# Optimization experiments

Measured on AMD Instinct MI355X. Metric: run time of the kernel, lower is better.

## Reference

```python
import jax, jax.numpy as jnp
import numpy as np

UNITS = 2048

def _cat_complex(Wr, Wi):
    # real-matrix representation of complex matmul: [[Wr, -Wi], [Wi, Wr]]
    top = jnp.concatenate([Wr, -Wi], axis=-1)
    bot = jnp.concatenate([Wi, Wr], axis=-1)
    return jnp.concatenate([top, bot], axis=0)

def _hard_sigmoid(x):
    return jnp.clip(0.2 * x + 0.5, 0.0, 1.0)

def setup_inputs() -> dict:
    key = jax.random.key(0)
    ks = jax.random.split(key, 8)
    B, IN2, U3 = 1024, 4096, 3 * UNITS
    s_in = 1.0 / np.sqrt(IN2)
    s_h = 1.0 / np.sqrt(2 * UNITS)
    return {
        "inputs": jax.random.normal(ks[0], (B, IN2), jnp.float32),
        "h_tm1": jax.random.normal(ks[1], (B, 2 * UNITS), jnp.float32),
        "real_kernel": jax.random.normal(ks[2], (IN2 // 2, U3), jnp.float32) * s_in,
        "imaginary_kernel": jax.random.normal(ks[3], (IN2 // 2, U3), jnp.float32) * s_in,
        "real_recurrent_kernel": jax.random.normal(ks[4], (UNITS, U3), jnp.float32) * s_h,
        "imaginary_recurrent_kernel": jax.random.normal(ks[5], (UNITS, U3), jnp.float32) * s_h,
        "real_bias": jax.random.normal(ks[6], (U3,), jnp.float32) * 0.01,
        "imaginary_bias": jax.random.normal(ks[7], (U3,), jnp.float32) * 0.01,
    }

def reference(inputs, h_tm1, real_kernel, imaginary_kernel,
              real_recurrent_kernel, imaginary_recurrent_kernel,
              real_bias, imaginary_bias):
    u = UNITS
    # per-gate complex kernels in real [[Wr,-Wi],[Wi,Wr]] form
    Kz = _cat_complex(real_kernel[:, :u], imaginary_kernel[:, :u])
    Kr = _cat_complex(real_kernel[:, u:2 * u], imaginary_kernel[:, u:2 * u])
    Kh = _cat_complex(real_kernel[:, 2 * u:], imaginary_kernel[:, 2 * u:])
    Rz = _cat_complex(real_recurrent_kernel[:, :u], imaginary_recurrent_kernel[:, :u])
    Rr = _cat_complex(real_recurrent_kernel[:, u:2 * u], imaginary_recurrent_kernel[:, u:2 * u])
    Rh = _cat_complex(real_recurrent_kernel[:, 2 * u:], imaginary_recurrent_kernel[:, 2 * u:])
    bz = jnp.concatenate([real_bias[:u], imaginary_bias[:u]])
    br = jnp.concatenate([real_bias[u:2 * u], imaginary_bias[u:2 * u]])
    bh = jnp.concatenate([real_bias[2 * u:], imaginary_bias[2 * u:]])
    # implementation=1, reset_after=False, no dropout
    x_z = inputs @ Kz + bz
    x_r = inputs @ Kr + br
    x_h = inputs @ Kh + bh
    z = _hard_sigmoid(x_z + h_tm1 @ Rz)
    r = _hard_sigmoid(x_r + h_tm1 @ Rr)
    hh = jnp.tanh(x_h + (r * h_tm1) @ Rh)
    h = z * h_tm1 + (1.0 - z) * hh
    return h
```

## Files before the change

### kernel.cpp

```cpp
#include <hip/hip_runtime.h>

typedef _Float16 half8  __attribute__((ext_vector_type(8)));
typedef _Float16 half4v __attribute__((ext_vector_type(4)));
typedef _Float16 half2v __attribute__((ext_vector_type(2)));
typedef float    float4v __attribute__((ext_vector_type(4)));

__device__ __forceinline__ float hsig(float x) {
  return fminf(fmaxf(fmaf(x, 0.2f, 0.5f), 0.0f), 1.0f);
}

__global__ __launch_bounds__(256) void cvt_pair(const float* __restrict__ src,
                                                _Float16* __restrict__ d1,
                                                _Float16* __restrict__ d2) {
  int i = blockIdx.x * blockDim.x + threadIdx.x;
  int base = i * 4;
  int j = base & 4095;
  float s = (j < 2048) ? -1.0f : 1.0f;
  float4 v = *(const float4*)&src[base];
  half4v h1 = {(_Float16)v.x, (_Float16)v.y, (_Float16)v.z, (_Float16)v.w};
  half4v h2 = {(_Float16)(s * v.x), (_Float16)(s * v.y), (_Float16)(s * v.z), (_Float16)(s * v.w)};
  *(half4v*)&d1[base] = h1;
  *(half4v*)&d2[base] = h2;
}

__global__ __launch_bounds__(256) void transpose_cast(
    const float* __restrict__ s0, const float* __restrict__ s1,
    const float* __restrict__ s2, const float* __restrict__ s3,
    _Float16* __restrict__ d0, _Float16* __restrict__ d1m,
    _Float16* __restrict__ d2m, _Float16* __restrict__ d3m)
{
  __shared__ float tile[64][65];
  const float* srcs[4] = {s0, s1, s2, s3};
  _Float16*    dsts[4] = {d0, d1m, d2m, d3m};
  const float* src = srcs[blockIdx.z];
  _Float16*    dst = dsts[blockIdx.z];

  const int tid = threadIdx.x;
  const int k0 = blockIdx.x * 64;
  const int j0 = blockIdx.y * 64;

  const int tx = tid & 63, ty = tid >> 6;
#pragma unroll
  for (int r = 0; r < 64; r += 4)
    tile[r + ty][tx] = src[(size_t)(k0 + r + ty) * 6144 + j0 + tx];
  __syncthreads();

  const int txk = (tid & 31) * 2;
  const int tyn = tid >> 5;
#pragma unroll
  for (int r = 0; r < 64; r += 8) {
    int jl = r + tyn;
    half2v p = {(_Float16)tile[txk][jl], (_Float16)tile[txk + 1][jl]};
    *(half2v*)&dst[(size_t)(j0 + jl) * 2048 + k0 + txk] = p;
  }
}

__global__ __launch_bounds__(256) void rgate(const _Float16* __restrict__ xacc,
                                             const float* __restrict__ h,
                                             _Float16* __restrict__ A1r,
                                             _Float16* __restrict__ A2r) {
  int i = blockIdx.x * blockDim.x + threadIdx.x;
  int base = i * 4;
  int m = base >> 12;
  int j = base & 4095;
  float s = (j < 2048) ? -1.0f : 1.0f;
  half4v rp = *(const half4v*)&xacc[(size_t)m * 12288 + 4096 + j];
  float4 hv = *(const float4*)&h[base];
  float p0 = hsig((float)rp[0]) * hv.x;
  float p1 = hsig((float)rp[1]) * hv.y;
  float p2 = hsig((float)rp[2]) * hv.z;
  float p3 = hsig((float)rp[3]) * hv.w;
  half4v o1 = {(_Float16)p0, (_Float16)p1, (_Float16)p2, (_Float16)p3};
  half4v o2 = {(_Float16)(s * p0), (_Float16)(s * p1), (_Float16)(s * p2), (_Float16)(s * p3)};
  *(half4v*)&A1r[base] = o1;
  *(half4v*)&A2r[base] = o2;
}

__global__ __launch_bounds__(256) void combine(const _Float16* __restrict__ xacc,
                                               const _Float16* __restrict__ P0,
                                               const _Float16* __restrict__ P1,
                                               const float* __restrict__ h,
                                               float* __restrict__ out) {
  int i = blockIdx.x * blockDim.x + threadIdx.x;
  int base = i * 4;
  int m = base >> 12;
  int j = base & 4095;
  half4v zv = *(const half4v*)&xacc[(size_t)m * 12288 + j];
  half4v xh = *(const half4v*)&xacc[(size_t)m * 12288 + 8192 + j];
  half4v p0 = *(const half4v*)&P0[base];
  half4v p1 = *(const half4v*)&P1[base];
  float4 hv = *(const float4*)&h[base];
  float4 o;
  {
    float z = hsig((float)zv[0]); float t = tanhf((float)xh[0] + (float)p0[0] + (float)p1[0]);
    o.x = z * hv.x + (1.0f - z) * t;
  }
  {
    float z = hsig((float)zv[1]); float t = tanhf((float)xh[1] + (float)p0[1] + (float)p1[1]);
    o.y = z * hv.y + (1.0f - z) * t;
  }
  {
    float z = hsig((float)zv[2]); float t = tanhf((float)xh[2] + (float)p0[2] + (float)p1[2]);
    o.z = z * hv.z + (1.0f - z) * t;
  }
  {
    float z = hsig((float)zv[3]); float t = tanhf((float)xh[3] + (float)p0[3] + (float)p1[3]);
    o.w = z * hv.w + (1.0f - z) * t;
  }
  *(float4*)&out[base] = o;
}

template<int FINAL>
__global__ __launch_bounds__(256, 3) void gemm_big(
    const _Float16* __restrict__ Ax1, const _Float16* __restrict__ Ax2,
    const _Float16* __restrict__ Ah1, const _Float16* __restrict__ Ah2,
    const _Float16* __restrict__ WKr, const _Float16* __restrict__ WKi,
    const _Float16* __restrict__ WRr, const _Float16* __restrict__ WRi,
    _Float16* __restrict__ xacc,
    _Float16* __restrict__ P0, _Float16* __restrict__ P1,
    const float* __restrict__ rbias, const float* __restrict__ ibias)
{
  __shared__ __align__(16) _Float16 lds[16384];
  const int tid  = threadIdx.x;
  const int lane = tid & 63;
  const int wave = tid >> 6;
  const int quad = lane >> 4;
  const int r16  = lane & 15;
  const int wm = (wave >> 1) * 64;
  const int wn = (wave & 1) * 64;
  const int mbase = blockIdx.y * 128;
  const int nbase = blockIdx.x * 128;

  const int  gate   = nbase >> 12;
  const bool hi     = (nbase & 2048) != 0;
  const int  jprime = nbase & 2047;

  int nph;
  const _Float16* pA[4];
  const _Float16* pB[4];
  if (FINAL) {
    nph = 1;
    const _Float16* Ax = hi ? Ax2 : Ax1;
    const _Float16* BL = hi ? WKi : WKr;
    const _Float16* BH = hi ? WKr : WKi;
    if (blockIdx.z == 0) {
      pA[0] = Ax + (size_t)mbase * 4096;
      pB[0] = BL + (size_t)jprime * 2048;
    } else {
      pA[0] = Ax + (size_t)mbase * 4096 + 2048;
      pB[0] = BH + (size_t)jprime * 2048;
    }
  } else {
    const size_t browK = (size_t)(gate * 2048 + jprime) * 2048;
    const _Float16* Ax = hi ? Ax2 : Ax1;
    const _Float16* KL = hi ? WKi : WKr;
    const _Float16* KH = hi ? WKr : WKi;
    pA[0] = Ax + (size_t)mbase * 4096;      pB[0] = KL + browK;
    pA[1] = pA[0] + 2048;                   pB[1] = KH + browK;
    if (gate < 2) {
      nph = 4;
      const _Float16* Ah = hi ? Ah2 : Ah1;
      const _Float16* RL = hi ? WRi : WRr;
      const _Float16* RH = hi ? WRr : WRi;
      pA[2] = Ah + (size_t)mbase * 4096;    pB[2] = RL + browK;
      pA[3] = pA[2] + 2048;                 pB[3] = RH + browK;
    } else {
      nph = 2;
    }
  }

  float4v acc[4][4];
#pragma unroll
  for (int i = 0; i < 4; ++i)
#pragma unroll
    for (int j = 0; j < 4; ++j) acc[i][j] = (float4v){0.f, 0.f, 0.f, 0.f};

  int offA[4], offB[4], ldsA[4], ldsB[4];
#pragma unroll
  for (int i = 0; i < 4; ++i) {
    int c = i * 256 + tid;
    int row = c >> 3;
    int sw = (c & 7) ^ (row & 7);
    offA[i] = row * 4096 + sw * 8;
    offB[i] = row * 2048 + sw * 8;
    ldsA[i] = c * 8;
    ldsB[i] = 8192 + c * 8;
  }

#pragma unroll 1
  for (int p = 0; p < 4; ++p) {
    if (p >= nph) break;
    const _Float16* Ab = pA[p];
    const _Float16* Bb = pB[p];
#pragma unroll 1
    for (int it = 0; it < 32; ++it) {
#pragma unroll
      for (int i = 0; i < 4; ++i)
        __builtin_amdgcn_global_load_lds(
            (__attribute__((address_space(1))) void*)(Ab + offA[i]),
            (__attribute__((address_space(3))) void*)&lds[ldsA[i]], 16, 0, 0);
#pragma unroll
      for (int i = 0; i < 4; ++i)
        __builtin_amdgcn_global_load_lds(
            (__attribute__((address_space(1))) void*)(Bb + offB[i]),
            (__attribute__((address_space(3))) void*)&lds[ldsB[i]], 16, 0, 0);
      Ab += 64;
      Bb += 64;
      __syncthreads();
#pragma unroll
      for (int ks = 0; ks < 2; ++ks) {
        half8 af[4], bf[4];
        int akg = ks * 4 + quad;
#pragma unroll
        for (int t = 0; t < 4; ++t) {
          int arow = wm + t * 16 + r16;
          af[t] = *(const half8*)&lds[(arow * 8 + (akg ^ (arow & 7))) * 8];
          int brow = wn + t * 16 + r16;
          bf[t] = *(const half8*)&lds[8192 + (brow * 8 + (akg ^ (brow & 7))) * 8];
        }
#pragma unroll
        for (int mt = 0; mt < 4; ++mt)
#pragma unroll
          for (int nt = 0; nt < 4; ++nt)
            acc[mt][nt] = __builtin_amdgcn_mfma_f32_16x16x32_f16(af[mt], bf[nt], acc[mt][nt], 0, 0, 0);
      }
      __syncthreads();
    }
  }

  const int mrow0 = mbase + wm + quad * 4;
  const int ncol0 = nbase + wn + r16;
  if (!FINAL) {
#pragma unroll
    for (int nt = 0; nt < 4; ++nt) {
      int n = ncol0 + nt * 16;
      int g = n >> 12, j = n & 4095;
      float b = (j < 2048) ? rbias[g * 2048 + j] : ibias[g * 2048 + j - 2048];
#pragma unroll
      for (int mt = 0; mt < 4; ++mt)
#pragma unroll
        for (int e = 0; e < 4; ++e) {
          int m = mrow0 + mt * 16 + e;
          xacc[(size_t)m * 12288 + n] = (_Float16)(acc[mt][nt][e] + b);
        }
    }
  } else {
    _Float16* P = blockIdx.z ? P1 : P0;
#pragma unroll
    for (int nt = 0; nt < 4; ++nt) {
      int n = ncol0 + nt * 16;
#pragma unroll
      for (int mt = 0; mt < 4; ++mt)
#pragma unroll
        for (int e = 0; e < 4; ++e) {
          int m = mrow0 + mt * 16 + e;
          P[(size_t)m * 4096 + n] = (_Float16)acc[mt][nt][e];
        }
    }
  }
}

extern "C" void kernel_launch(void* const* d_in, const int* in_sizes, int n_in,
                              void* d_out, int out_size, void* d_ws, size_t ws_size,
                              hipStream_t stream) {
  const float* inputs = (const float*)d_in[0];
  const float* h_tm1  = (const float*)d_in[1];
  const float* rk     = (const float*)d_in[2];
  const float* ik     = (const float*)d_in[3];
  const float* rrk    = (const float*)d_in[4];
  const float* irk    = (const float*)d_in[5];
  const float* rb     = (const float*)d_in[6];
  const float* ib     = (const float*)d_in[7];
  float* out = (float*)d_out;

  char* ws = (char*)d_ws;
  _Float16* WrK  = (_Float16*)(ws + 0);
  _Float16* WiK  = (_Float16*)(ws + 25165824);
  _Float16* WrR  = (_Float16*)(ws + 50331648);
  _Float16* WiR  = (_Float16*)(ws + 75497472);
  _Float16* A1x  = (_Float16*)(ws + 100663296);
  _Float16* A2x  = (_Float16*)(ws + 109051904);
  _Float16* A1h  = (_Float16*)(ws + 117440512);
  _Float16* A2h  = (_Float16*)(ws + 125829120);
  _Float16* xacc = (_Float16*)(ws + 134217728);
  _Float16* A1r  = A1x;
  _Float16* A2r  = A2x;
  _Float16* P0   = A1h;
  _Float16* P1   = A2h;

  cvt_pair<<<4096, 256, 0, stream>>>(inputs, A1x, A2x);
  cvt_pair<<<4096, 256, 0, stream>>>(h_tm1, A1h, A2h);
  transpose_cast<<<dim3(32, 96, 4), 256, 0, stream>>>(rk, ik, rrk, irk, WrK, WiK, WrR, WiR);
  gemm_big<0><<<dim3(96, 8), 256, 0, stream>>>(A1x, A2x, A1h, A2h, WrK, WiK, WrR, WiR,
                                               xacc, nullptr, nullptr, rb, ib);
  rgate<<<4096, 256, 0, stream>>>(xacc, h_tm1, A1r, A2r);
  gemm_big<1><<<dim3(32, 8, 2), 256, 0, stream>>>(A1r, A2r, nullptr, nullptr,
                                                  WrR + (size_t)4096 * 2048,
                                                  WiR + (size_t)4096 * 2048,
                                                  nullptr, nullptr, nullptr, P0, P1,
                                                  nullptr, nullptr);
  combine<<<4096, 256, 0, stream>>>(xacc, P0, P1, h_tm1, out);
}
```

Baseline: 512.9 us.

## Replace first fused GEMM with 128x256-tile 512-thread kernel using direct-to-LDS loads

Adds a new gemm256 kernel for the input-plus-recurrent z/r/h GEMM. It uses 128x256 output tiles with 8 waves and a 4-buffer LDS ring filled by global_load_lds with two stages in flight, and raises MFMA wave priority. The larger tiles cut the grid from 96x8 to 48x8 blocks and increase operand reuse per tile. In exchange it needs 96KB of dynamic LDS per block, which limits occupancy, and the ring and waitcnt logic is handwritten.

```diff
diff --git a/kernel.cpp b/kernel.cpp
--- a/kernel.cpp
+++ b/kernel.cpp
@@ -108,6 +108,144 @@
     o.w = z * hv.w + (1.0f - z) * t;
   }
   *(float4*)&out[base] = o;
+}
+
+__global__ __launch_bounds__(512, 2) void gemm256(
+    const _Float16* __restrict__ Ax1, const _Float16* __restrict__ Ax2,
+    const _Float16* __restrict__ Ah1, const _Float16* __restrict__ Ah2,
+    const _Float16* __restrict__ WKr, const _Float16* __restrict__ WKi,
+    const _Float16* __restrict__ WRr, const _Float16* __restrict__ WRi,
+    _Float16* __restrict__ xacc,
+    const float* __restrict__ rbias, const float* __restrict__ ibias)
+{
+  extern __shared__ __align__(16) _Float16 smem[];
+  const int tid  = threadIdx.x;
+  const int lane = tid & 63;
+  const int wave = tid >> 6;
+  const int quad = lane >> 4;
+  const int r16  = lane & 15;
+  const int wm = (wave >> 2) * 64;
+  const int wn = (wave & 3) * 64;
+  const int mbase = blockIdx.y * 128;
+  const int nbase = blockIdx.x * 256;
+
+  const int  gate   = nbase >> 12;
+  const bool hi     = (nbase & 2048) != 0;
+  const int  jprime = nbase & 2047;
+
+  int nph;
+  const _Float16 *pA0, *pA1, *pA2, *pA3;
+  const _Float16 *pB0, *pB1, *pB2, *pB3;
+  {
+    const size_t browK = (size_t)(gate * 2048 + jprime) * 2048;
+    const _Float16* Ax = hi ? Ax2 : Ax1;
+    const _Float16* KL = hi ? WKi : WKr;
+    const _Float16* KH = hi ? WKr : WKi;
+    pA0 = Ax + (size_t)mbase * 4096;      pB0 = KL + browK;
+    pA1 = pA0 + 2048;                     pB1 = KH + browK;
+    if (gate < 2) {
+      nph = 4;
+      const _Float16* Ah = hi ? Ah2 : Ah1;
+      const _Float16* RL = hi ? WRi : WRr;
+      const _Float16* RH = hi ? WRr : WRi;
+      pA2 = Ah + (size_t)mbase * 4096;    pB2 = RL + browK;
+      pA3 = pA2 + 2048;                   pB3 = RH + browK;
+    } else {
+      nph = 2;
+      pA2 = pA0; pB2 = pB0; pA3 = pA0; pB3 = pB0;
+    }
+  }
+  const int NS = nph * 64;
+
+  const int arow_s = tid >> 2;
+  const int ag     = (tid & 3) ^ ((arow_s ^ (arow_s >> 2)) & 3);
+  const size_t aoff = (size_t)arow_s * 4096 + ag * 8;
+  const int aldsd   = tid * 8;
+
+  const int brow_s0 = tid >> 2;
+  const int bg0     = (tid & 3) ^ ((brow_s0 ^ (brow_s0 >> 2)) & 3);
+  const size_t boff0 = (size_t)brow_s0 * 2048 + bg0 * 8;
+  const int bldsd0   = tid * 8;
+  const int brow_s1 = brow_s0 + 128;
+  const int bg1     = (tid & 3) ^ ((brow_s1 ^ (brow_s1 >> 2)) & 3);
+  const size_t boff1 = (size_t)brow_s1 * 2048 + bg1 * 8;
+  const int bldsd1   = (tid + 512) * 8;
+
+#define STAGE(S2) do {                                                          \
+    int p2_ = (S2) >> 6;                                                        \
+    int kof_ = ((S2) & 63) * 32;                                                \
+    int bb_ = (S2) & 3;                                                         \
+    const _Float16* As_ = p2_ == 0 ? pA0 : p2_ == 1 ? pA1 : p2_ == 2 ? pA2 : pA3; \
+    const _Float16* Bs_ = p2_ == 0 ? pB0 : p2_ == 1 ? pB1 : p2_ == 2 ? pB2 : pB3; \
+    __builtin_amdgcn_global_load_lds(                                           \
+        (__attribute__((address_space(1))) void*)(As_ + aoff + kof_),           \
+        (__attribute__((address_space(3))) void*)&smem[bb_ * 4096 + aldsd], 16, 0, 0); \
+    __builtin_amdgcn_global_load_lds(                                           \
+        (__attribute__((address_space(1))) void*)(Bs_ + boff0 + kof_),          \
+        (__attribute__((address_space(3))) void*)&smem[16384 + bb_ * 8192 + bldsd0], 16, 0, 0); \
+    __builtin_amdgcn_global_load_lds(                                           \
+        (__attribute__((address_space(1))) void*)(Bs_ + boff1 + kof_),          \
+        (__attribute__((address_space(3))) void*)&smem[16384 + bb_ * 8192 + bldsd1], 16, 0, 0); \
+  } while (0)
+
+  float4v acc[4][4];
+#pragma unroll
+  for (int i = 0; i < 4; ++i)
+#pragma unroll
+    for (int j = 0; j < 4; ++j) acc[i][j] = (float4v){0.f, 0.f, 0.f, 0.f};
+
+  STAGE(0);
+  STAGE(1);
+
+#pragma unroll 1
+  for (int s = 0; s < NS; ++s) {
+    if (s + 2 < NS) {
+      STAGE(s + 2);
+      asm volatile("s_waitcnt vmcnt(6)" ::: "memory");
+    } else if (s + 1 < NS) {
+      asm volatile("s_waitcnt vmcnt(3)" ::: "memory");
+    } else {
+      asm volatile("s_waitcnt vmcnt(0)" ::: "memory");
+    }
+    __builtin_amdgcn_s_barrier();
+    asm volatile("" ::: "memory");
+
+    const int b = s & 3;
+    half8 af[4], bf[4];
+#pragma unroll
+    for (int t = 0; t < 4; ++t) {
+      int arow = wm + t * 16 + r16;
+      af[t] = *(const half8*)&smem[b * 4096 +
+                 (arow * 4 + (quad ^ ((arow ^ (arow >> 2)) & 3))) * 8];
+      int brow = wn + t * 16 + r16;
+      bf[t] = *(const half8*)&smem[16384 + b * 8192 +
+                 (brow * 4 + (quad ^ ((brow ^ (brow >> 2)) & 3))) * 8];
+    }
+    __builtin_amdgcn_s_setprio(1);
+#pragma unroll
+    for (int mt = 0; mt < 4; ++mt)
+#pragma unroll
+      for (int nt = 0; nt < 4; ++nt)
+        acc[mt][nt] = __builtin_amdgcn_mfma_f32_16x16x32_f16(af[mt], bf[nt], acc[mt][nt], 0, 0, 0);
+    __builtin_amdgcn_s_setprio(0);
+  }
+#undef STAGE
+
+  const int mrow0 = mbase + wm + quad * 4;
+  const int ncol0 = nbase + wn + r16;
+#pragma unroll
+  for (int nt = 0; nt < 4; ++nt) {
+    int n = ncol0 + nt * 16;
+    int g = n >> 12, j = n & 4095;
+    float bia = (j < 2048) ? rbias[g * 2048 + j] : ibias[g * 2048 + j - 2048];
+#pragma unroll
+    for (int mt = 0; mt < 4; ++mt)
+#pragma unroll
+      for (int e = 0; e < 4; ++e) {
+        int m = mrow0 + mt * 16 + e;
+        xacc[(size_t)m * 12288 + n] = (_Float16)(acc[mt][nt][e] + bia);
+      }
+  }
 }
 
 template<int FINAL>
@@ -291,8 +429,8 @@
   cvt_pair<<<4096, 256, 0, stream>>>(inputs, A1x, A2x);
   cvt_pair<<<4096, 256, 0, stream>>>(h_tm1, A1h, A2h);
   transpose_cast<<<dim3(32, 96, 4), 256, 0, stream>>>(rk, ik, rrk, irk, WrK, WiK, WrR, WiR);
-  gemm_big<0><<<dim3(96, 8), 256, 0, stream>>>(A1x, A2x, A1h, A2h, WrK, WiK, WrR, WiR,
-                                               xacc, nullptr, nullptr, rb, ib);
+  gemm256<<<dim3(48, 8), 512, 98304, stream>>>(A1x, A2x, A1h, A2h, WrK, WiK, WrR, WiR,
+                                               xacc, rb, ib);
   rgate<<<4096, 256, 0, stream>>>(xacc, h_tm1, A1r, A2r);
   gemm_big<1><<<dim3(32, 8, 2), 256, 0, stream>>>(A1r, A2r, nullptr, nullptr,
                                                   WrR + (size_t)4096 * 2048,
```

Result: slower. 611.0 us (+19.1%).

## Use Gauss three-multiplication complex matmul with split-K recurrent GEMM

Applied to the files above, without the earlier changes.

The four-real-GEMM complex product becomes Gauss's three-product form. Prep kernels build (r-i), (r+i) and i weight planes and r, i, r+i activation planes, and each GEMM tile runs three K-phases. The shared product is kept in fp16 registers and folded into both the real and imaginary outputs. The aim is to cut MFMA work by about a quarter; the fp16 stash and the extra sums add rounding error. The candidate GEMM is also split four ways over K with partial outputs summed in the combine kernel, and workgroup IDs are remapped for locality.

```diff
diff --git a/kernel.cpp b/kernel.cpp
--- a/kernel.cpp
+++ b/kernel.cpp
@@ -9,117 +9,149 @@
   return fminf(fmaxf(fmaf(x, 0.2f, 0.5f), 0.0f), 1.0f);
 }
 
-__global__ __launch_bounds__(256) void cvt_pair(const float* __restrict__ src,
-                                                _Float16* __restrict__ d1,
-                                                _Float16* __restrict__ d2) {
-  int i = blockIdx.x * blockDim.x + threadIdx.x;
+__device__ __forceinline__ half2v pk2(float a, float b) {
+  half2v r; r[0] = (_Float16)a; r[1] = (_Float16)b; return r;
+}
+
+
+__global__ __launch_bounds__(256) void prep_a(const float* __restrict__ x,
+                                              const float* __restrict__ h,
+                                              _Float16* __restrict__ PXr, _Float16* __restrict__ PXi,
+                                              _Float16* __restrict__ PXs, _Float16* __restrict__ PHr,
+                                              _Float16* __restrict__ PHi, _Float16* __restrict__ PHs) {
+  int i = blockIdx.x * 256 + threadIdx.x;
+  const float* src; _Float16 *Pr, *Pi, *Ps;
+  if (blockIdx.y == 0) { src = x; Pr = PXr; Pi = PXi; Ps = PXs; }
+  else                 { src = h; Pr = PHr; Pi = PHi; Ps = PHs; }
   int base = i * 4;
-  int j = base & 4095;
-  float s = (j < 2048) ? -1.0f : 1.0f;
-  float4 v = *(const float4*)&src[base];
-  half4v h1 = {(_Float16)v.x, (_Float16)v.y, (_Float16)v.z, (_Float16)v.w};
-  half4v h2 = {(_Float16)(s * v.x), (_Float16)(s * v.y), (_Float16)(s * v.z), (_Float16)(s * v.w)};
-  *(half4v*)&d1[base] = h1;
-  *(half4v*)&d2[base] = h2;
-}
-
-__global__ __launch_bounds__(256) void transpose_cast(
-    const float* __restrict__ s0, const float* __restrict__ s1,
-    const float* __restrict__ s2, const float* __restrict__ s3,
-    _Float16* __restrict__ d0, _Float16* __restrict__ d1m,
-    _Float16* __restrict__ d2m, _Float16* __restrict__ d3m)
-{
-  __shared__ float tile[64][65];
-  const float* srcs[4] = {s0, s1, s2, s3};
-  _Float16*    dsts[4] = {d0, d1m, d2m, d3m};
-  const float* src = srcs[blockIdx.z];
-  _Float16*    dst = dsts[blockIdx.z];
-
+  int m = base >> 11, j = base & 2047;
+  float4 a  = *(const float4*)&src[(size_t)m * 4096 + j];
+  float4 bv = *(const float4*)&src[(size_t)m * 4096 + 2048 + j];
+  size_t o = (size_t)m * 2048 + j;
+  half4v hr, hi2, hs;
+  hr[0]=(_Float16)a.x;  hr[1]=(_Float16)a.y;  hr[2]=(_Float16)a.z;  hr[3]=(_Float16)a.w;
+  hi2[0]=(_Float16)bv.x; hi2[1]=(_Float16)bv.y; hi2[2]=(_Float16)bv.z; hi2[3]=(_Float16)bv.w;
+  hs[0]=(_Float16)(a.x+bv.x); hs[1]=(_Float16)(a.y+bv.y);
+  hs[2]=(_Float16)(a.z+bv.z); hs[3]=(_Float16)(a.w+bv.w);
+  *(half4v*)&Pr[o] = hr;
+  *(half4v*)&Pi[o] = hi2;
+  *(half4v*)&Ps[o] = hs;
+}
+
+__global__ __launch_bounds__(256) void transpose_cast3(
+    const float* __restrict__ rkK, const float* __restrict__ ikK,
+    const float* __restrict__ rkR, const float* __restrict__ ikR,
+    _Float16* __restrict__ WdK, _Float16* __restrict__ WsK, _Float16* __restrict__ WiK,
+    _Float16* __restrict__ WdR, _Float16* __restrict__ WsR, _Float16* __restrict__ WiR) {
+  __shared__ float tr[64][65];
+  __shared__ float ti[64][65];
+  const float* rs  = blockIdx.z ? rkR : rkK;
+  const float* is2 = blockIdx.z ? ikR : ikK;
+  _Float16* Wd = blockIdx.z ? WdR : WdK;
+  _Float16* Ws = blockIdx.z ? WsR : WsK;
+  _Float16* Wi = blockIdx.z ? WiR : WiK;
   const int tid = threadIdx.x;
   const int k0 = blockIdx.x * 64;
   const int j0 = blockIdx.y * 64;
-
   const int tx = tid & 63, ty = tid >> 6;
 #pragma unroll
-  for (int r = 0; r < 64; r += 4)
-    tile[r + ty][tx] = src[(size_t)(k0 + r + ty) * 6144 + j0 + tx];
+  for (int r = 0; r < 64; r += 4) {
+    size_t so = (size_t)(k0 + r + ty) * 6144 + j0 + tx;
+    tr[r + ty][tx] = rs[so];
+    ti[r + ty][tx] = is2[so];
+  }
   __syncthreads();
-
   const int txk = (tid & 31) * 2;
   const int tyn = tid >> 5;
 #pragma unroll
   for (int r = 0; r < 64; r += 8) {
     int jl = r + tyn;
-    half2v p = {(_Float16)tile[txk][jl], (_Float16)tile[txk + 1][jl]};
-    *(half2v*)&dst[(size_t)(j0 + jl) * 2048 + k0 + txk] = p;
-  }
-}
-
-__global__ __launch_bounds__(256) void rgate(const _Float16* __restrict__ xacc,
-                                             const float* __restrict__ h,
-                                             _Float16* __restrict__ A1r,
-                                             _Float16* __restrict__ A2r) {
-  int i = blockIdx.x * blockDim.x + threadIdx.x;
-  int base = i * 4;
-  int m = base >> 12;
-  int j = base & 4095;
-  float s = (j < 2048) ? -1.0f : 1.0f;
-  half4v rp = *(const half4v*)&xacc[(size_t)m * 12288 + 4096 + j];
-  float4 hv = *(const float4*)&h[base];
-  float p0 = hsig((float)rp[0]) * hv.x;
-  float p1 = hsig((float)rp[1]) * hv.y;
-  float p2 = hsig((float)rp[2]) * hv.z;
-  float p3 = hsig((float)rp[3]) * hv.w;
-  half4v o1 = {(_Float16)p0, (_Float16)p1, (_Float16)p2, (_Float16)p3};
-  half4v o2 = {(_Float16)(s * p0), (_Float16)(s * p1), (_Float16)(s * p2), (_Float16)(s * p3)};
-  *(half4v*)&A1r[base] = o1;
-  *(half4v*)&A2r[base] = o2;
-}
-
-__global__ __launch_bounds__(256) void combine(const _Float16* __restrict__ xacc,
-                                               const _Float16* __restrict__ P0,
-                                               const _Float16* __restrict__ P1,
-                                               const float* __restrict__ h,
-                                               float* __restrict__ out) {
-  int i = blockIdx.x * blockDim.x + threadIdx.x;
-  int base = i * 4;
-  int m = base >> 12;
-  int j = base & 4095;
-  half4v zv = *(const half4v*)&xacc[(size_t)m * 12288 + j];
-  half4v xh = *(const half4v*)&xacc[(size_t)m * 12288 + 8192 + j];
-  half4v p0 = *(const half4v*)&P0[base];
-  half4v p1 = *(const half4v*)&P1[base];
-  float4 hv = *(const float4*)&h[base];
-  float4 o;
-  {
-    float z = hsig((float)zv[0]); float t = tanhf((float)xh[0] + (float)p0[0] + (float)p1[0]);
-    o.x = z * hv.x + (1.0f - z) * t;
-  }
-  {
-    float z = hsig((float)zv[1]); float t = tanhf((float)xh[1] + (float)p0[1] + (float)p1[1]);
-    o.y = z * hv.y + (1.0f - z) * t;
-  }
-  {
-    float z = hsig((float)zv[2]); float t = tanhf((float)xh[2] + (float)p0[2] + (float)p1[2]);
-    o.z = z * hv.z + (1.0f - z) * t;
-  }
-  {
-    float z = hsig((float)zv[3]); float t = tanhf((float)xh[3] + (float)p0[3] + (float)p1[3]);
-    o.w = z * hv.w + (1.0f - z) * t;
-  }
-  *(float4*)&out[base] = o;
-}
-
-template<int FINAL>
-__global__ __launch_bounds__(256, 3) void gemm_big(
-    const _Float16* __restrict__ Ax1, const _Float16* __restrict__ Ax2,
-    const _Float16* __restrict__ Ah1, const _Float16* __restrict__ Ah2,
-    const _Float16* __restrict__ WKr, const _Float16* __restrict__ WKi,
-    const _Float16* __restrict__ WRr, const _Float16* __restrict__ WRi,
-    _Float16* __restrict__ xacc,
+    float r0 = tr[txk][jl], r1 = tr[txk + 1][jl];
+    float i0 = ti[txk][jl], i1 = ti[txk + 1][jl];
+    size_t dof = (size_t)(j0 + jl) * 2048 + k0 + txk;
+    *(half2v*)&Wd[dof] = pk2(r0 - i0, r1 - i1);
+    *(half2v*)&Ws[dof] = pk2(r0 + i0, r1 + i1);
+    *(half2v*)&Wi[dof] = pk2(i0, i1);
+  }
+}
+
+__device__ __forceinline__ void run_phase(const _Float16* Ab, const _Float16* Bb, int nit,
+                                          _Float16* lds, int tid, int wm, int wn,
+                                          int quad, int r16, float4v (&acc)[4][4]) {
+  int off[4], ldsA[4], ldsB[4];
+#pragma unroll
+  for (int i = 0; i < 4; ++i) {
+    int c = i * 256 + tid;
+    int row = c >> 3;
+    int sw = (c & 7) ^ (row & 7);
+    off[i]  = row * 2048 + sw * 8;
+    ldsA[i] = c * 8;
+    ldsB[i] = 8192 + c * 8;
+  }
+#pragma unroll 1
+  for (int it = 0; it < nit; ++it) {
+#pragma unroll
+    for (int i = 0; i < 4; ++i)
+      __builtin_amdgcn_global_load_lds(
+          (__attribute__((address_space(1))) void*)(Ab + off[i]),
+          (__attribute__((address_space(3))) void*)&lds[ldsA[i]], 16, 0, 0);
+#pragma unroll
+    for (int i = 0; i < 4; ++i)
+      __builtin_amdgcn_global_load_lds(
+          (__attribute__((address_space(1))) void*)(Bb + off[i]),
+          (__attribute__((address_space(3))) void*)&lds[ldsB[i]], 16, 0, 0);
+    Ab += 64;
+    Bb += 64;
+    __syncthreads();
+#pragma unroll
+    for (int ks = 0; ks < 2; ++ks) {
+      half8 af[4], bf[4];
+      int akg = ks * 4 + quad;
+#pragma unroll
+      for (int t = 0; t < 4; ++t) {
+        int arow = wm + t * 16 + r16;
+        af[t] = *(const half8*)&lds[(arow * 8 + (akg ^ (arow & 7))) * 8];
+        int brow = wn + t * 16 + r16;
+        bf[t] = *(const half8*)&lds[8192 + (brow * 8 + (akg ^ (brow & 7))) * 8];
+      }
+#pragma unroll
+      for (int mt = 0; mt < 4; ++mt)
+#pragma unroll
+        for (int nt = 0; nt < 4; ++nt)
+          acc[mt][nt] = __builtin_amdgcn_mfma_f32_16x16x32_f16(af[mt], bf[nt], acc[mt][nt], 0, 0, 0);
+    }
+    __syncthreads();
+  }
+}
+
+__device__ __forceinline__ void write_tile(_Float16* __restrict__ dst, int ldc, int colbase,
+    int mrow0, int ncol0, const float4v (&acc)[4][4], const half2v (&stash)[4][4][2],
+    float ssign, const float* __restrict__ bias, int bbase) {
+#pragma unroll
+  for (int nt = 0; nt < 4; ++nt) {
+    int nl = ncol0 + nt * 16;
+    float bv = bias ? bias[bbase + nl] : 0.0f;
+#pragma unroll
+    for (int mt = 0; mt < 4; ++mt)
+#pragma unroll
+      for (int e = 0; e < 4; ++e) {
+        float sv = (float)stash[mt][nt][e >> 1][e & 1];
+        int m = mrow0 + mt * 16 + e;
+        dst[(size_t)m * ldc + colbase + nl] = (_Float16)(acc[mt][nt][e] + ssign * sv + bv);
+      }
+  }
+}
+
+template<int MODE>
+__global__ __launch_bounds__(256, 3) void gemm_gauss(
+    const _Float16* __restrict__ WdK, const _Float16* __restrict__ WsK, const _Float16* __restrict__ WiK,
+    const _Float16* __restrict__ WdR, const _Float16* __restrict__ WsR, const _Float16* __restrict__ WiR,
+    const _Float16* __restrict__ PXr, const _Float16* __restrict__ PXi, const _Float16* __restrict__ PXs,
+    const _Float16* __restrict__ PHr, const _Float16* __restrict__ PHi, const _Float16* __restrict__ PHs,
+    _Float16* __restrict__ xaccX, _Float16* __restrict__ xaccH,
     _Float16* __restrict__ P0, _Float16* __restrict__ P1,
-    const float* __restrict__ rbias, const float* __restrict__ ibias)
-{
+    _Float16* __restrict__ P2, _Float16* __restrict__ P3,
+    const float* __restrict__ rbias, const float* __restrict__ ibias) {
   __shared__ __align__(16) _Float16 lds[16384];
   const int tid  = threadIdx.x;
   const int lane = tid & 63;
@@ -128,136 +160,161 @@
   const int r16  = lane & 15;
   const int wm = (wave >> 1) * 64;
   const int wn = (wave & 1) * 64;
-  const int mbase = blockIdx.y * 128;
-  const int nbase = blockIdx.x * 128;
-
-  const int  gate   = nbase >> 12;
-  const bool hi     = (nbase & 2048) != 0;
-  const int  jprime = nbase & 2047;
-
-  int nph;
-  const _Float16* pA[4];
-  const _Float16* pB[4];
-  if (FINAL) {
-    nph = 1;
-    const _Float16* Ax = hi ? Ax2 : Ax1;
-    const _Float16* BL = hi ? WKi : WKr;
-    const _Float16* BH = hi ? WKr : WKi;
-    if (blockIdx.z == 0) {
-      pA[0] = Ax + (size_t)mbase * 4096;
-      pB[0] = BL + (size_t)jprime * 2048;
+
+  const int NWG = MODE ? 512 : 640;
+  int b = blockIdx.x;
+  int wid = (b & 7) * (NWG >> 3) + (b >> 3);
+
+  int gate, jb, row, nit;
+  const _Float16 *A0, *A1, *A2, *B0, *B1, *B2;
+  _Float16* dst; int ldc, colRe, bbase;
+  const float *rb2, *ib2;
+
+  if (MODE == 0) {
+    nit = 32;
+    int side;
+    if (wid < 512) { gate = wid >> 8; side = (wid >> 7) & 1; jb = (wid >> 3) & 15; row = wid & 7; }
+    else { int t = wid - 512; gate = 2; side = 0; jb = (t >> 3) & 15; row = t & 7; }
+    size_t boff = (size_t)(gate * 2048 + jb * 128) * 2048;
+    size_t aoff = (size_t)(row * 128) * 2048;
+    if (side == 0) {
+      A0 = PXs + aoff; A1 = PXr + aoff; A2 = PXi + aoff;
+      B0 = WiK + boff; B1 = WdK + boff; B2 = WsK + boff;
+      dst = xaccX; ldc = 12288;
+      rb2 = rbias; ib2 = ibias;
     } else {
-      pA[0] = Ax + (size_t)mbase * 4096 + 2048;
-      pB[0] = BH + (size_t)jprime * 2048;
+      A0 = PHs + aoff; A1 = PHr + aoff; A2 = PHi + aoff;
+      B0 = WiR + boff; B1 = WdR + boff; B2 = WsR + boff;
+      dst = xaccH; ldc = 8192;
+      rb2 = nullptr; ib2 = nullptr;
     }
+    colRe = gate * 4096 + jb * 128;
+    bbase = gate * 2048 + jb * 128;
   } else {
-    const size_t browK = (size_t)(gate * 2048 + jprime) * 2048;
-    const _Float16* Ax = hi ? Ax2 : Ax1;
-    const _Float16* KL = hi ? WKi : WKr;
-    const _Float16* KH = hi ? WKr : WKi;
-    pA[0] = Ax + (size_t)mbase * 4096;      pB[0] = KL + browK;
-    pA[1] = pA[0] + 2048;                   pB[1] = KH + browK;
-    if (gate < 2) {
-      nph = 4;
-      const _Float16* Ah = hi ? Ah2 : Ah1;
-      const _Float16* RL = hi ? WRi : WRr;
-      const _Float16* RH = hi ? WRr : WRi;
-      pA[2] = Ah + (size_t)mbase * 4096;    pB[2] = RL + browK;
-      pA[3] = pA[2] + 2048;                 pB[3] = RH + browK;
-    } else {
-      nph = 2;
+    nit = 8;
+    int z = wid >> 7; int t = wid & 127;
+    jb = (t >> 3) & 15; row = t & 7;
+    int koff = z * 512;
+    size_t boff = (size_t)(4096 + jb * 128) * 2048 + koff;
+    size_t aoff = (size_t)(row * 128) * 2048 + koff;
+    A0 = PXs + aoff; A1 = PXr + aoff; A2 = PXi + aoff;
+    B0 = WiR + boff; B1 = WdR + boff; B2 = WsR + boff;
+    dst = (z == 0) ? P0 : (z == 1) ? P1 : (z == 2) ? P2 : P3;
+    ldc = 4096; colRe = jb * 128; bbase = 0;
+    gate = 0; rb2 = nullptr; ib2 = nullptr;
+  }
+
+  float4v acc[4][4];
+#pragma unroll
+  for (int i = 0; i < 4; ++i)
+#pragma unroll
+    for (int j = 0; j < 4; ++j) acc[i][j] = (float4v){0.f, 0.f, 0.f, 0.f};
+
+  run_phase(A0, B0, nit, lds, tid, wm, wn, quad, r16, acc);
+  half2v stash[4][4][2];
+#pragma unroll
+  for (int mt = 0; mt < 4; ++mt)
+#pragma unroll
+    for (int nt = 0; nt < 4; ++nt) {
+      stash[mt][nt][0] = pk2(acc[mt][nt][0], acc[mt][nt][1]);
+      stash[mt][nt][1] = pk2(acc[mt][nt][2], acc[mt][nt][3]);
+      acc[mt][nt] = (float4v){0.f, 0.f, 0.f, 0.f};
     }
-  }
-
-  float4v acc[4][4];
-#pragma unroll
-  for (int i = 0; i < 4; ++i)
-#pragma unroll
-    for (int j = 0; j < 4; ++j) acc[i][j] = (float4v){0.f, 0.f, 0.f, 0.f};
-
-  int offA[4], offB[4], ldsA[4], ldsB[4];
-#pragma unroll
-  for (int i = 0; i < 4; ++i) {
-    int c = i * 256 + tid;
-    int row = c >> 3;
-    int sw = (c & 7) ^ (row & 7);
-    offA[i] = row * 4096 + sw * 8;
-    offB[i] = row * 2048 + sw * 8;
-    ldsA[i] = c * 8;
-    ldsB[i] = 8192 + c * 8;
-  }
-
-#pragma unroll 1
-  for (int p = 0; p < 4; ++p) {
-    if (p >= nph) break;
-    const _Float16* Ab = pA[p];
-    const _Float16* Bb = pB[p];
-#pragma unroll 1
-    for (int it = 0; it < 32; ++it) {
-#pragma unroll
-      for (int i = 0; i < 4; ++i)
-        __builtin_amdgcn_global_load_lds(
-            (__attribute__((address_space(1))) void*)(Ab + offA[i]),
-            (__attribute__((address_space(3))) void*)&lds[ldsA[i]], 16, 0, 0);
-#pragma unroll
-      for (int i = 0; i < 4; ++i)
-        __builtin_amdgcn_global_load_lds(
-            (__attribute__((address_space(1))) void*)(Bb + offB[i]),
-            (__attribute__((address_space(3))) void*)&lds[ldsB[i]], 16, 0, 0);
-      Ab += 64;
-      Bb += 64;
-      __syncthreads();
-#pragma unroll
-      for (int ks = 0; ks < 2; ++ks) {
-        half8 af[4], bf[4];
-        int akg = ks * 4 + quad;
-#pragma unroll
-        for (int t = 0; t < 4; ++t) {
-          int arow = wm + t * 16 + r16;
-          af[t] = *(const half8*)&lds[(arow * 8 + (akg ^ (arow & 7))) * 8];
-          int brow = wn + t * 16 + r16;
-          bf[t] = *(const half8*)&lds[8192 + (brow * 8 + (akg ^ (brow & 7))) * 8];
-        }
-#pragma unroll
-        for (int mt = 0; mt < 4; ++mt)
-#pragma unroll
-          for (int nt = 0; nt < 4; ++nt)
-            acc[mt][nt] = __builtin_amdgcn_mfma_f32_16x16x32_f16(af[mt], bf[nt], acc[mt][nt], 0, 0, 0);
-      }
-      __syncthreads();
-    }
-  }
-
-  const int mrow0 = mbase + wm + quad * 4;
-  const int ncol0 = nbase + wn + r16;
-  if (!FINAL) {
-#pragma unroll
-    for (int nt = 0; nt < 4; ++nt) {
-      int n = ncol0 + nt * 16;
-      int g = n >> 12, j = n & 4095;
-      float b = (j < 2048) ? rbias[g * 2048 + j] : ibias[g * 2048 + j - 2048];
-#pragma unroll
-      for (int mt = 0; mt < 4; ++mt)
-#pragma unroll
-        for (int e = 0; e < 4; ++e) {
-          int m = mrow0 + mt * 16 + e;
-          xacc[(size_t)m * 12288 + n] = (_Float16)(acc[mt][nt][e] + b);
-        }
-    }
-  } else {
-    _Float16* P = blockIdx.z ? P1 : P0;
-#pragma unroll
-    for (int nt = 0; nt < 4; ++nt) {
-      int n = ncol0 + nt * 16;
-#pragma unroll
-      for (int mt = 0; mt < 4; ++mt)
-#pragma unroll
-        for (int e = 0; e < 4; ++e) {
-          int m = mrow0 + mt * 16 + e;
-          P[(size_t)m * 4096 + n] = (_Float16)acc[mt][nt][e];
-        }
-    }
-  }
+
+  const int mrow0 = row * 128 + wm + quad * 4;
+  const int ncol0 = wn + r16;
+
+  run_phase(A1, B1, nit, lds, tid, wm, wn, quad, r16, acc);
+  write_tile(dst, ldc, colRe, mrow0, ncol0, acc, stash, 1.0f, rb2, bbase);
+
+#pragma unroll
+  for (int mt = 0; mt < 4; ++mt)
+#pragma unroll
+    for (int nt = 0; nt < 4; ++nt) acc[mt][nt] = (float4v){0.f, 0.f, 0.f, 0.f};
+
+  run_phase(A2, B2, nit, lds, tid, wm, wn, quad, r16, acc);
+  write_tile(dst, ldc, colRe + 2048, mrow0, ncol0, acc, stash, -1.0f, ib2, bbase);
+}
+
+__global__ __launch_bounds__(256) void rgate3(const _Float16* __restrict__ xaccX,
+                                              const _Float16* __restrict__ xaccH,
+                                              const float* __restrict__ h,
+                                              _Float16* __restrict__ PRr,
+                                              _Float16* __restrict__ PRi,
+                                              _Float16* __restrict__ PRs) {
+  int i = blockIdx.x * 256 + threadIdx.x;
+  int base = i * 4;
+  int m = base >> 11, j = base & 2047;
+  half4v a1 = *(const half4v*)&xaccX[(size_t)m * 12288 + 4096 + j];
+  half4v a2 = *(const half4v*)&xaccH[(size_t)m * 8192 + 4096 + j];
+  half4v b1 = *(const half4v*)&xaccX[(size_t)m * 12288 + 4096 + 2048 + j];
+  half4v b2 = *(const half4v*)&xaccH[(size_t)m * 8192 + 4096 + 2048 + j];
+  float4 h1 = *(const float4*)&h[(size_t)m * 4096 + j];
+  float4 h2 = *(const float4*)&h[(size_t)m * 4096 + 2048 + j];
+  float p1[4], p2[4];
+  p1[0] = hsig((float)a1[0] + (float)a2[0]) * h1.x;
+  p1[1] = hsig((float)a1[1] + (float)a2[1]) * h1.y;
+  p1[2] = hsig((float)a1[2] + (float)a2[2]) * h1.z;
+  p1[3] = hsig((float)a1[3] + (float)a2[3]) * h1.w;
+  p2[0] = hsig((float)b1[0] + (float)b2[0]) * h2.x;
+  p2[1] = hsig((float)b1[1] + (float)b2[1]) * h2.y;
+  p2[2] = hsig((float)b1[2] + (float)b2[2]) * h2.z;
+  p2[3] = hsig((float)b1[3] + (float)b2[3]) * h2.w;
+  size_t o = (size_t)m * 2048 + j;
+  half4v orr, oi, os;
+#pragma unroll
+  for (int e = 0; e < 4; ++e) {
+    orr[e] = (_Float16)p1[e];
+    oi[e]  = (_Float16)p2[e];
+    os[e]  = (_Float16)(p1[e] + p2[e]);
+  }
+  *(half4v*)&PRr[o] = orr;
+  *(half4v*)&PRi[o] = oi;
+  *(half4v*)&PRs[o] = os;
+}
+
+__global__ __launch_bounds__(256) void combine4(const _Float16* __restrict__ xaccX,
+                                                const _Float16* __restrict__ xaccH,
+                                                const _Float16* __restrict__ P0,
+                                                const _Float16* __restrict__ P1,
+                                                const _Float16* __restrict__ P2,
+                                                const _Float16* __restrict__ P3,
+                                                const float* __restrict__ h,
+                                                float* __restrict__ out) {
+  int i = blockIdx.x * 256 + threadIdx.x;
+  int base = i * 4;
+  int m = base >> 12;
+  int j = base & 4095;
+  half4v zx = *(const half4v*)&xaccX[(size_t)m * 12288 + j];
+  half4v zh = *(const half4v*)&xaccH[(size_t)m * 8192 + j];
+  half4v xh = *(const half4v*)&xaccX[(size_t)m * 12288 + 8192 + j];
+  half4v p0 = *(const half4v*)&P0[base];
+  half4v p1 = *(const half4v*)&P1[base];
+  half4v p2 = *(const half4v*)&P2[base];
+  half4v p3 = *(const half4v*)&P3[base];
+  float4 hv = *(const float4*)&h[base];
+  float4 o;
+  {
+    float z = hsig((float)zx[0] + (float)zh[0]);
+    float t = tanhf((float)xh[0] + (float)p0[0] + (float)p1[0] + (float)p2[0] + (float)p3[0]);
+    o.x = z * hv.x + (1.0f - z) * t;
+  }
+  {
+    float z = hsig((float)zx[1] + (float)zh[1]);
+    float t = tanhf((float)xh[1] + (float)p0[1] + (float)p1[1] + (float)p2[1] + (float)p3[1]);
+    o.y = z * hv.y + (1.0f - z) * t;
+  }
+  {
+    float z = hsig((float)zx[2] + (float)zh[2]);
+    float t = tanhf((float)xh[2] + (float)p0[2] + (float)p1[2] + (float)p2[2] + (float)p3[2]);
+    o.z = z * hv.z + (1.0f - z) * t;
+  }
+  {
+    float z = hsig((float)zx[3] + (float)zh[3]);
+    float t = tanhf((float)xh[3] + (float)p0[3] + (float)p1[3] + (float)p2[3] + (float)p3[3]);
+    o.w = z * hv.w + (1.0f - z) * t;
+  }
+  *(float4*)&out[base] = o;
 }
 
 extern "C" void kernel_launch(void* const* d_in, const int* in_sizes, int n_in,
@@ -274,30 +331,39 @@
   float* out = (float*)d_out;
 
   char* ws = (char*)d_ws;
-  _Float16* WrK  = (_Float16*)(ws + 0);
-  _Float16* WiK  = (_Float16*)(ws + 25165824);
-  _Float16* WrR  = (_Float16*)(ws + 50331648);
-  _Float16* WiR  = (_Float16*)(ws + 75497472);
-  _Float16* A1x  = (_Float16*)(ws + 100663296);
-  _Float16* A2x  = (_Float16*)(ws + 109051904);
-  _Float16* A1h  = (_Float16*)(ws + 117440512);
-  _Float16* A2h  = (_Float16*)(ws + 125829120);
-  _Float16* xacc = (_Float16*)(ws + 134217728);
-  _Float16* A1r  = A1x;
-  _Float16* A2r  = A2x;
-  _Float16* P0   = A1h;
-  _Float16* P1   = A2h;
-
-  cvt_pair<<<4096, 256, 0, stream>>>(inputs, A1x, A2x);
-  cvt_pair<<<4096, 256, 0, stream>>>(h_tm1, A1h, A2h);
-  transpose_cast<<<dim3(32, 96, 4), 256, 0, stream>>>(rk, ik, rrk, irk, WrK, WiK, WrR, WiR);
-  gemm_big<0><<<dim3(96, 8), 256, 0, stream>>>(A1x, A2x, A1h, A2h, WrK, WiK, WrR, WiR,
-                                               xacc, nullptr, nullptr, rb, ib);
-  rgate<<<4096, 256, 0, stream>>>(xacc, h_tm1, A1r, A2r);
-  gemm_big<1><<<dim3(32, 8, 2), 256, 0, stream>>>(A1r, A2r, nullptr, nullptr,
-                                                  WrR + (size_t)4096 * 2048,
-                                                  WiR + (size_t)4096 * 2048,
-                                                  nullptr, nullptr, nullptr, P0, P1,
-                                                  nullptr, nullptr);
-  combine<<<4096, 256, 0, stream>>>(xacc, P0, P1, h_tm1, out);
-}
+  _Float16* WdK = (_Float16*)(ws + 0);
+  _Float16* WsK = (_Float16*)(ws + 25165824);
+  _Float16* WiK = (_Float16*)(ws + 50331648);
+  _Float16* WdR = (_Float16*)(ws + 75497472);
+  _Float16* WsR = (_Float16*)(ws + 100663296);
+  _Float16* WiR = (_Float16*)(ws + 125829120);
+  _Float16* PXr = (_Float16*)(ws + 150994944);
+  _Float16* PXi = (_Float16*)(ws + 155189248);
+  _Float16* PXs = (_Float16*)(ws + 159383552);
+  _Float16* PHr = (_Float16*)(ws + 163577856);
+  _Float16* PHi = (_Float16*)(ws + 167772160);
+  _Float16* PHs = (_Float16*)(ws + 171966464);
+  _Float16* xaccX = (_Float16*)(ws + 176160768);
+  _Float16* xaccH = (_Float16*)(ws + 201326592);
+  _Float16* PRr = PXr;
+  _Float16* PRi = PXi;
+  _Float16* PRs = PXs;
+  _Float16* P0  = (_Float16*)(ws + 0);
+  _Float16* P1  = (_Float16*)(ws + 8388608);
+  _Float16* P2  = (_Float16*)(ws + 16777216);
+  _Float16* P3  = (_Float16*)(ws + 25165824);
+
+  prep_a<<<dim3(2048, 2), 256, 0, stream>>>(inputs, h_tm1, PXr, PXi, PXs, PHr, PHi, PHs);
+  transpose_cast3<<<dim3(32, 96, 2), 256, 0, stream>>>(rk, ik, rrk, irk,
+                                                       WdK, WsK, WiK, WdR, WsR, WiR);
+  gemm_gauss<0><<<640, 256, 0, stream>>>(WdK, WsK, WiK, WdR, WsR, WiR,
+                                         PXr, PXi, PXs, PHr, PHi, PHs,
+                                         xaccX, xaccH,
+                                         nullptr, nullptr, nullptr, nullptr, rb, ib);
+  rgate3<<<2048, 256, 0, stream>>>(xaccX, xaccH, h_tm1, PRr, PRi, PRs);
+  gemm_gauss<1><<<512, 256, 0, stream>>>(WdK, WsK, WiK, WdR, WsR, WiR,
+                                         PRr, PRi, PRs, nullptr, nullptr, nullptr,
+                                         nullptr, nullptr, P0, P1, P2, P3,
+                                         nullptr, nullptr);
+  combine4<<<4096, 256, 0, stream>>>(xaccX, xaccH, P0, P1, P2, P3, h_tm1, out);
+}
```

New measurement: 551.5 us. 7.5% more time.
